# Optimization experiments

Measured on AMD Instinct MI355X. Metric: run time of the kernel, lower is better.

Reference implementation:

```python
import jax, jax.numpy as jnp
import numpy as np

K = 20
EPS = 1e-5
NEG_SLOPE = 0.2


def _knn(x):
    # x: (B, C, N) -> idx of K nearest (largest negative sq dist): (B, N, K)
    inner = -2.0 * jnp.einsum('bcn,bcm->bnm', x, x)
    xx = jnp.sum(x * x, axis=1)  # (B, N)
    pd = -xx[:, :, None] - inner - xx[:, None, :]
    return jax.lax.top_k(pd, K)[1]


def _graph_feature(x):
    # x: (B, C, N) -> (B, 2C, N, K) edge features cat(nbr - center, center)
    idx = _knn(x)                              # (B, N, K)
    xt = jnp.swapaxes(x, 1, 2)                 # (B, N, C)
    nbr = jax.vmap(lambda f, i: f[i])(xt, idx)  # (B, N, K, C)
    center = xt[:, :, None, :]
    feat = jnp.concatenate([nbr - center, jnp.broadcast_to(center, nbr.shape)], axis=-1)
    return jnp.transpose(feat, (0, 3, 1, 2))


def _bn(x, g, b, m, v):
    # inference-mode batchnorm over channel axis 1
    shp = [1] * x.ndim
    shp[1] = -1
    scale = (g / jnp.sqrt(v + EPS)).reshape(shp)
    return (x - m.reshape(shp)) * scale + b.reshape(shp)


def _lrelu(x):
    return jnp.where(x >= 0, x, NEG_SLOPE * x)


def setup_inputs() -> dict:
    key = jax.random.key(0)
    ks = jax.random.split(key, 16)
    d = {
        'x': jax.random.normal(ks[0], (4, 2, 4096), jnp.float32),
        'W1': jax.random.normal(ks[1], (64, 4), jnp.float32),
        'g1': jax.random.uniform(ks[2], (64,), jnp.float32),
        'b1': jax.random.normal(ks[3], (64,), jnp.float32),
        'm1': jnp.zeros((64,), jnp.float32),
        'v1': jnp.ones((64,), jnp.float32),
        'W2': jax.random.normal(ks[4], (64, 128), jnp.float32),
        'g2': jax.random.uniform(ks[5], (64,), jnp.float32),
        'b2': jax.random.normal(ks[6], (64,), jnp.float32),
        'm2': jnp.zeros((64,), jnp.float32),
        'v2': jnp.ones((64,), jnp.float32),
        'W5': jax.random.normal(ks[7], (128, 128), jnp.float32),
        'g5': jax.random.uniform(ks[8], (128,), jnp.float32),
        'b5': jax.random.normal(ks[9], (128,), jnp.float32),
        'm5': jnp.zeros((128,), jnp.float32),
        'v5': jnp.ones((128,), jnp.float32),
        'W6': jax.random.normal(ks[10], (256, 256), jnp.float32),
        'g6': jax.random.uniform(ks[11], (256,), jnp.float32),
        'b6': jax.random.normal(ks[12], (256,), jnp.float32),
        'm6': jnp.zeros((256,), jnp.float32),
        'v6': jnp.ones((256,), jnp.float32),
        'W9': jax.random.normal(ks[13], (1, 256), jnp.float32),
    }
    return d


def reference(x, W1, g1, b1, m1, v1, W2, g2, b2, m2, v2,
              W5, g5, b5, m5, v5, W6, g6, b6, m6, v6, W9):
    B, _, N = x.shape
    # EdgeConv 1
    f = _graph_feature(x)                                     # (B, 4, N, K)
    h = _lrelu(_bn(jnp.einsum('bcnk,oc->bonk', f, W1), g1, b1, m1, v1))
    x1 = jnp.max(h, axis=-1)                                  # (B, 64, N)
    # EdgeConv 2 (graph rebuilt in feature space)
    f = _graph_feature(x1)                                    # (B, 128, N, K)
    h = _lrelu(_bn(jnp.einsum('bcnk,oc->bonk', f, W2), g2, b2, m2, v2))
    x2 = jnp.max(h, axis=-1)                                  # (B, 64, N)
    xc = jnp.concatenate([x1, x2], axis=1)                    # (B, 128, N)
    # conv5 (1x1 conv1d) + global max pool
    h5 = _lrelu(_bn(jnp.einsum('bcn,oc->bon', xc, W5), g5, b5, m5, v5))  # (B, 128, N)
    gmax = jnp.max(h5, axis=-1)                               # (B, 128)
    rep = jnp.broadcast_to(gmax[:, :, None], (B, gmax.shape[1], N))
    cat = jnp.concatenate([rep, xc], axis=1)                  # (B, 256, N)
    # conv6 (dropout is identity in eval) then conv9
    h6 = _lrelu(_bn(jnp.einsum('bcn,oc->bon', cat, W6), g6, b6, m6, v6))
    out = jnp.einsum('bcn,oc->bon', h6, W9)                   # (B, 1, N)
    return out.reshape(B, N)
```

## Files before the change

### kernel.cpp

```cpp
#include <hip/hip_runtime.h>
#include <math.h>

#define NEGINF (-INFINITY)
constexpr int Np = 4096;
constexpr int Kn = 20;
constexpr float EPSf = 1e-5f;
constexpr float SLOPE = 0.2f;

typedef __bf16 bf16x8 __attribute__((ext_vector_type(8)));
typedef float f32x4 __attribute__((ext_vector_type(4)));
typedef unsigned long long ull;
typedef unsigned int u32;
typedef unsigned short u16;

__global__ __launch_bounds__(512, 2) void k1_knn1_edge1(
    const float* __restrict__ x, const float* __restrict__ W1,
    const float* __restrict__ g1, const float* __restrict__ b1,
    const float* __restrict__ m1, const float* __restrict__ v1,
    float* __restrict__ x1, __bf16* __restrict__ x1h, __bf16* __restrict__ x1l,
    float* __restrict__ xx2)
{
  __shared__ u32 smem32[16000];
  float* pk1  = (float*)smem32;
  u16*   pi1  = (u16*)((char*)smem32 + 32768);
  u32*   thrK = (u32*)((char*)smem32 + 49152);
  u32*   ku   = smem32;
  u16*   ki   = (u16*)((char*)smem32 + 40960);
  u16*   midx = (u16*)((char*)smem32 + 61440);
  float* nbr  = (float*)smem32;

  const int b = blockIdx.y;
  const int n0 = blockIdx.x * 64;
  const int tid = threadIdx.x;
  const int w = tid >> 6, L = tid & 63;
  const float* __restrict__ xr = x + (size_t)b*2*Np;
  const float* __restrict__ yr = xr + Np;

  const int n = n0 + L;
  const float px = xr[n], py = yr[n];

  if (tid < 64) thrK[tid] = 0xFFFFFFFFu;
  __syncthreads();

  ull kv[20];
#pragma unroll
  for (int s = 0; s < 20; ++s) kv[s] = 0ull;
  u32 u_cut = 0xFFFFFFFFu;
  int cnt = 0;

  auto flushK = [&]() {
#pragma unroll 1
    for (int f0 = 0; f0 < 16; f0 += 4) {
      if (__all(f0 >= cnt)) break;
      float fv[4]; u32 ji[4];
#pragma unroll
      for (int u = 0; u < 4; ++u) {
        fv[u] = pk1[(f0+u)*512 + tid];
        ji[u] = pi1[(f0+u)*512 + tid];
      }
#pragma unroll
      for (int u = 0; u < 4; ++u) {
        int f = f0 + u;
        ull key = (((ull)(~__float_as_uint(fv[u]))) << 32) | (u32)~ji[u];
        if (f < cnt && key > kv[19]) {
          ull ck = key;
#pragma unroll
          for (int s = 0; s < 20; ++s) {
            bool sw = ck > kv[s];
            ull tv = kv[s];
            kv[s] = sw ? ck : kv[s];
            ck = sw ? tv : ck;
          }
        }
      }
    }
    cnt = 0;
    u32 uc = ~(u32)(kv[19] >> 32);
    atomicMin(&thrK[L], uc);
    u_cut = thrK[L];
  };

  const int base = w * 512;
#pragma unroll 1
  for (int j0 = base; j0 < base + 512; j0 += 16) {
    {
      u32 hs = thrK[L];
      u_cut = hs < u_cut ? hs : u_cut;
    }
#pragma unroll
    for (int c = 0; c < 4; ++c) {
      float4 xv = *reinterpret_cast<const float4*>(xr + j0 + c*4);
      float4 yv = *reinterpret_cast<const float4*>(yr + j0 + c*4);
      const float xs[4] = {xv.x, xv.y, xv.z, xv.w};
      const float ys[4] = {yv.x, yv.y, yv.z, yv.w};
#pragma unroll
      for (int r = 0; r < 4; ++r) {
        float dx = xs[r] - px, dy = ys[r] - py;
        float s = dx*dx + dy*dy;
        u32 ub = __float_as_uint(s);
        if (ub <= u_cut) {
          pk1[cnt*512 + tid] = s;
          pi1[cnt*512 + tid] = (u16)(j0 + c*4 + r);
          ++cnt;
        }
      }
      if (__any(cnt >= 13)) flushK();
    }
  }
  flushK();

  __syncthreads();
#pragma unroll
  for (int k = 0; k < Kn; ++k) {
    ku[((size_t)w*64 + L)*20 + k] = (u32)(kv[k] >> 32);
    ki[((size_t)w*64 + L)*20 + k] = (u16)~(u32)kv[k];
  }
  __syncthreads();

  if (tid < 64) {
    const int p = tid;
    u32 hk_[8]; u16 hj_[8]; int pc[8];
#pragma unroll
    for (int q = 0; q < 8; ++q) {
      size_t bi = ((size_t)q*64 + p)*20;
      hk_[q] = ku[bi]; hj_[q] = ki[bi]; pc[q] = 0;
    }
    for (int k = 0; k < Kn; ++k) {
      u32 bk = hk_[0]; u16 bj = hj_[0]; int sel = 0;
#pragma unroll
      for (int q = 1; q < 8; ++q) {
        bool better = (hk_[q] > bk) || (hk_[q] == bk && hj_[q] < bj);
        if (better) { bk = hk_[q]; bj = hj_[q]; sel = q; }
      }
      midx[p*20 + k] = bj;
      int np_ = ++pc[sel];
      size_t bi = ((size_t)sel*64 + p)*20;
      hk_[sel] = (np_ < 20) ? ku[bi + np_] : 0u;
      hj_[sel] = (np_ < 20) ? ki[bi + np_] : (u16)0xFFFF;
    }
  }
  __syncthreads();

  for (int i = tid; i < 64*Kn; i += 512) {
    int j = midx[i];
    nbr[i*2]     = xr[j];
    nbr[i*2 + 1] = yr[j];
  }
  __syncthreads();

  const int o = L;
  const float4 w1v = reinterpret_cast<const float4*>(W1)[o];
  const float sc = g1[o] / sqrtf(v1[o] + EPSf);
  const float mo = m1[o], bo = b1[o];

  for (int pi = 0; pi < 8; ++pi) {
    const int p = w*8 + pi;
    const int np = n0 + p;
    const float cx0 = xr[np], cx1 = yr[np];
    const float cterm = (w1v.z - w1v.x)*cx0 + (w1v.w - w1v.y)*cx1;
    float xm = NEGINF;
#pragma unroll
    for (int k = 0; k < Kn; ++k) {
      float2 nv = *reinterpret_cast<const float2*>(&nbr[(p*20 + k)*2]);
      float vv = w1v.x*nv.x + w1v.y*nv.y + cterm;
      float h = (vv - mo)*sc + bo;
      h = h >= 0.f ? h : SLOPE*h;
      xm = fmaxf(xm, h);
    }
    x1[(b*64 + o)*Np + np] = xm;
    __bf16 hb = (__bf16)xm;
    __bf16 lb = (__bf16)(xm - (float)hb);
    size_t tbase = ((size_t)b*Np + np)*64 + o;
    x1h[tbase] = hb;
    x1l[tbase] = lb;
    float s = xm*xm;
#pragma unroll
    for (int off = 1; off < 64; off <<= 1) s += __shfl_xor(s, off);
    if (L == 0) xx2[b*Np + np] = s;
  }
}

__global__ __launch_bounds__(256, 2) void k2_knn2(
    const __bf16* __restrict__ xh, const __bf16* __restrict__ xl,
    const float* __restrict__ xx2, int* __restrict__ idx2)
{
  __shared__ ull smem[5120];
  float* sxx = (float*)smem;
  float* pk  = (float*)((char*)smem + 16384);
  u16*   pi  = (u16*)((char*)smem + 31744);
  u32*   thr = (u32*)((char*)smem + 39424);

  const int b = blockIdx.y;
  const int n0 = blockIdx.x * 16;
  const int tid = threadIdx.x;
  const int w = tid >> 6, L = tid & 63;
  const int L15 = L & 15, quad = L >> 4;

  for (int j = tid*4; j < Np; j += 1024)
    *reinterpret_cast<float4*>(&sxx[j]) = *reinterpret_cast<const float4*>(&xx2[(size_t)b*Np + j]);
  if (tid < 16) thr[tid] = 0u;

  const __bf16* Rh = xh + ((size_t)b*Np + n0)*64;
  const __bf16* Rl = xl + ((size_t)b*Np + n0)*64;
  bf16x8 rh0 = *reinterpret_cast<const bf16x8*>(Rh + L15*64 +  0 + quad*8);
  bf16x8 rh1 = *reinterpret_cast<const bf16x8*>(Rh + L15*64 + 32 + quad*8);
  bf16x8 rl0 = *reinterpret_cast<const bf16x8*>(Rl + L15*64 +  0 + quad*8);
  bf16x8 rl1 = *reinterpret_cast<const bf16x8*>(Rl + L15*64 + 32 + quad*8);

  const __bf16* Cbh = xh + (size_t)b*Np*64;
  const __bf16* Cbl = xl + (size_t)b*Np*64;

  ull kv[20];
#pragma unroll
  for (int s = 0; s < 20; ++s) kv[s] = 0ull;
  float fthresh = NEGINF;
  int cnt = 0;

  __syncthreads();

  auto flush = [&]() {
#pragma unroll 1
    for (int f0 = 0; f0 < 15; f0 += 4) {
      if (__all(f0 >= cnt)) break;
      float fv[4]; u32 ji[4];
#pragma unroll
      for (int u = 0; u < 4; ++u) {
        fv[u] = pk[(f0+u)*256 + tid];
        ji[u] = pi[(f0+u)*256 + tid];
      }
#pragma unroll
      for (int u = 0; u < 4; ++u) {
        int f = f0 + u;
        u32 uu = __float_as_uint(fv[u]);
        u32 hk = uu ^ ((u32)((int)uu >> 31) | 0x80000000u);
        ull key = (((ull)hk) << 32) | (u32)~ji[u];
        if (f < cnt && key > kv[19]) {
          ull ck = key;
#pragma unroll
          for (int s = 0; s < 20; ++s) {
            bool sw = ck > kv[s];
            ull tv = kv[s];
            kv[s] = sw ? ck : kv[s];
            ck = sw ? tv : ck;
          }
        }
      }
    }
    cnt = 0;
    ull t = kv[19];
    ull t2 = __shfl_xor(t, 16); t = t2 > t ? t2 : t;
    t2 = __shfl_xor(t, 32);     t = t2 > t ? t2 : t;
    if (t != 0ull && quad == 0) atomicMax(&thr[L15], (u32)(t >> 32));
    u32 hs = thr[L15];
    if (hs != 0u) {
      u32 u = (hs >> 31) ? (hs ^ 0x80000000u) : ~hs;
      fthresh = fmaxf(fthresh, __uint_as_float(u));
    }
  };

#pragma unroll 1
  for (int t = 0; t < 16; ++t) {
    {
      u32 hs = thr[L15];
      if (hs != 0u) {
        u32 u = (hs >> 31) ? (hs ^ 0x80000000u) : ~hs;
        fthresh = fmaxf(fthresh, __uint_as_float(u));
      }
    }
    const int tt = w + t*4;
    const int colbase = tt * 64;
    const __bf16* ph = Cbh + (size_t)colbase*64;
    const __bf16* pl = Cbl + (size_t)colbase*64;
    bf16x8 AH[4][2], AL[4][2];
#pragma unroll
    for (int s = 0; s < 4; ++s) {
      AH[s][0] = *reinterpret_cast<const bf16x8*>(ph + (s*16 + L15)*64 +  0 + quad*8);
      AH[s][1] = *reinterpret_cast<const bf16x8*>(ph + (s*16 + L15)*64 + 32 + quad*8);
      AL[s][0] = *reinterpret_cast<const bf16x8*>(pl + (s*16 + L15)*64 +  0 + quad*8);
      AL[s][1] = *reinterpret_cast<const bf16x8*>(pl + (s*16 + L15)*64 + 32 + quad*8);
    }

    f32x4 acc[4];
#pragma unroll
    for (int s = 0; s < 4; ++s) {
      acc[s] = (f32x4){0.f, 0.f, 0.f, 0.f};
      acc[s] = __builtin_amdgcn_mfma_f32_16x16x32_bf16(AH[s][0], rh0, acc[s], 0, 0, 0);
      acc[s] = __builtin_amdgcn_mfma_f32_16x16x32_bf16(AH[s][1], rh1, acc[s], 0, 0, 0);
      acc[s] = __builtin_amdgcn_mfma_f32_16x16x32_bf16(AH[s][0], rl0, acc[s], 0, 0, 0);
      acc[s] = __builtin_amdgcn_mfma_f32_16x16x32_bf16(AH[s][1], rl1, acc[s], 0, 0, 0);
      acc[s] = __builtin_amdgcn_mfma_f32_16x16x32_bf16(AL[s][0], rh0, acc[s], 0, 0, 0);
      acc[s] = __builtin_amdgcn_mfma_f32_16x16x32_bf16(AL[s][1], rh1, acc[s], 0, 0, 0);
    }

#pragma unroll
    for (int s = 0; s < 4; ++s) {
      float4 xv = *reinterpret_cast<const float4*>(&sxx[colbase + s*16 + quad*4]);
      const float xvr[4] = {xv.x, xv.y, xv.z, xv.w};
#pragma unroll
      for (int r = 0; r < 4; ++r) {
        float e = 2.0f*acc[s][r] - xvr[r];
        if (e >= fthresh) {
          pk[cnt*256 + tid] = e;
          pi[cnt*256 + tid] = (u16)(colbase + s*16 + quad*4 + r);
          ++cnt;
        }
      }
      if (__any(cnt >= 12)) flush();
    }
  }
  flush();

  __syncthreads();
#pragma unroll
  for (int k = 0; k < Kn; ++k) smem[((size_t)w*64 + L)*20 + k] = kv[k];
  __syncthreads();

  if (tid < 16) {
    const int r = tid;
    ull h[16]; int pc[16];
#pragma unroll
    for (int i = 0; i < 16; ++i) {
      h[i] = smem[((size_t)(i>>2)*64 + (i&3)*16 + r)*20];
      pc[i] = 0;
    }
    size_t obase = ((size_t)b*Np + n0 + r)*Kn;
    for (int k = 0; k < Kn; ++k) {
      ull best = h[0]; int sel = 0;
#pragma unroll
      for (int i = 1; i < 16; ++i) if (h[i] > best) { best = h[i]; sel = i; }
      idx2[obase + k] = (int)~(u32)best;
      int np_ = ++pc[sel];
      h[sel] = (np_ < 20) ? smem[((size_t)(sel>>2)*64 + (sel&3)*16 + r)*20 + np_] : 0ull;
    }
  }
}

__global__ __launch_bounds__(256) void kY(
    const __bf16* __restrict__ xh, const __bf16* __restrict__ xl,
    const float* __restrict__ W2,
    const float* __restrict__ g2, const float* __restrict__ b2,
    const float* __restrict__ m2, const float* __restrict__ v2,
    float* __restrict__ Za, float* __restrict__ Cn)
{
  __shared__ float w2t[128*66];
  const int b = blockIdx.y;
  const int n0 = blockIdx.x * 16;
  const int tid = threadIdx.x;
  const int w = tid >> 6, L = tid & 63;

  for (int i = tid; i < 8192; i += 256) {
    int o = i >> 7, c = i & 127;
    w2t[c*66 + o] = W2[i];
  }
  __syncthreads();

  const float sc = g2[L] / sqrtf(v2[L] + EPSf);
  const float cc = b2[L] - m2[L]*sc;

  for (int pi = 0; pi < 4; ++pi) {
    const int n = n0 + w*4 + pi;
    const size_t base = ((size_t)b*Np + n)*64;
    const float xv = (float)xh[base + L] + (float)xl[base + L];
    float ya = 0.f, yb = 0.f;
#pragma unroll
    for (int c = 0; c < 64; ++c) {
      float xc = __shfl(xv, c);
      ya += w2t[c*66 + L] * xc;
      yb += w2t[(64 + c)*66 + L] * xc;
    }
    float za = sc * ya;
    Za[base + L] = za;
    Cn[base + L] = sc * yb + cc - za;
  }
}

__global__ __launch_bounds__(256, 2) void k3_gather(
    const float* __restrict__ Za, const float* __restrict__ Cn,
    const int* __restrict__ idx2, float* __restrict__ x2)
{
  const int b = blockIdx.y;
  const int tid = threadIdx.x;
  const int w = tid >> 6, L = tid & 63;
  const int n = blockIdx.x*4 + w;

  const int* ip = idx2 + ((size_t)b*Np + n)*Kn;
  int jreg = (L < Kn) ? ip[L] : 0;
  const float c = Cn[((size_t)b*Np + n)*64 + L];
  float xm = NEGINF;
#pragma unroll
  for (int k = 0; k < Kn; ++k) {
    int j = __shfl(jreg, k);
    float hh = Za[((size_t)b*Np + j)*64 + L] + c;
    hh = hh >= 0.f ? hh : SLOPE*hh;
    xm = fmaxf(xm, hh);
  }
  x2[(b*64 + L)*Np + n] = xm;
}

__global__ __launch_bounds__(512) void k4_conv5max(
    const float* __restrict__ x1, const float* __restrict__ x2,
    const float* __restrict__ W5,
    const float* __restrict__ g5, const float* __restrict__ b5,
    const float* __restrict__ m5, const float* __restrict__ v5,
    float* __restrict__ partials)
{
  const int b = blockIdx.y, nb = blockIdx.x;
  const int tid = threadIdx.x;
  const int p = tid & 63;
  const int g = __builtin_amdgcn_readfirstlane(tid >> 6);
  const int n = nb*64 + p;
  float xcr[128];
#pragma unroll
  for (int c = 0; c < 64; ++c) {
    xcr[c]    = x1[(b*64 + c)*Np + n];
    xcr[64+c] = x2[(b*64 + c)*Np + n];
  }
  for (int oi = 0; oi < 16; ++oi) {
    const int o = g*16 + oi;
    const float* wr = W5 + o*128;
    float dot = 0.f;
#pragma unroll
    for (int c = 0; c < 128; c += 4) {
      float4 wv = *reinterpret_cast<const float4*>(wr + c);
      dot += wv.x*xcr[c] + wv.y*xcr[c+1] + wv.z*xcr[c+2] + wv.w*xcr[c+3];
    }
    float hv = (dot - m5[o])*(g5[o]/sqrtf(v5[o]+EPSf)) + b5[o];
    hv = hv >= 0.f ? hv : SLOPE*hv;
#pragma unroll
    for (int off = 1; off < 64; off <<= 1) hv = fmaxf(hv, __shfl_xor(hv, off));
    if (p == 0) partials[(b*128 + o)*64 + nb] = hv;
  }
}

__global__ __launch_bounds__(256) void k5_reduce_t6(
    const float* __restrict__ partials, const float* __restrict__ W6,
    float* __restrict__ t6)
{
  __shared__ float sg[128];
  const int b = blockIdx.x;
  const int tid = threadIdx.x;
  if (tid < 128) {
    float m = NEGINF;
    for (int w = 0; w < 64; ++w) m = fmaxf(m, partials[(b*128 + tid)*64 + w]);
    sg[tid] = m;
  }
  __syncthreads();
  float a = 0.f;
#pragma unroll
  for (int c = 0; c < 128; c += 4) {
    float4 wv = *reinterpret_cast<const float4*>(W6 + tid*256 + c);
    a += wv.x*sg[c] + wv.y*sg[c+1] + wv.z*sg[c+2] + wv.w*sg[c+3];
  }
  t6[b*256 + tid] = a;
}

__global__ __launch_bounds__(512) void k6_conv6_out(
    const float* __restrict__ x1, const float* __restrict__ x2,
    const float* __restrict__ W6, const float* __restrict__ t6,
    const float* __restrict__ g6, const float* __restrict__ b6,
    const float* __restrict__ m6, const float* __restrict__ v6,
    const float* __restrict__ W9,
    float* __restrict__ out)
{
  __shared__ float red[8][64];
  const int b = blockIdx.y, nb = blockIdx.x;
  const int tid = threadIdx.x;
  const int p = tid & 63;
  const int g = __builtin_amdgcn_readfirstlane(tid >> 6);
  const int n = nb*64 + p;
  float xcr[128];
#pragma unroll
  for (int c = 0; c < 64; ++c) {
    xcr[c]    = x1[(b*64 + c)*Np + n];
    xcr[64+c] = x2[(b*64 + c)*Np + n];
  }
  float oacc = 0.f;
  for (int oi = 0; oi < 32; ++oi) {
    const int o = g*32 + oi;
    const float* wr = W6 + o*256 + 128;
    float dot = t6[b*256 + o];
#pragma unroll
    for (int c = 0; c < 128; c += 4) {
      float4 wv = *reinterpret_cast<const float4*>(wr + c);
      dot += wv.x*xcr[c] + wv.y*xcr[c+1] + wv.z*xcr[c+2] + wv.w*xcr[c+3];
    }
    float hv = (dot - m6[o])*(g6[o]/sqrtf(v6[o]+EPSf)) + b6[o];
    hv = hv >= 0.f ? hv : SLOPE*hv;
    oacc += W9[o]*hv;
  }
  red[g][p] = oacc;
  __syncthreads();
  if (tid < 64) {
    float s = 0.f;
#pragma unroll
    for (int q = 0; q < 8; ++q) s += red[q][tid];
    out[b*Np + nb*64 + tid] = s;
  }
}

extern "C" void kernel_launch(void* const* d_in, const int* in_sizes, int n_in,
                              void* d_out, int out_size, void* d_ws, size_t ws_size,
                              hipStream_t stream) {
  const float* x  = (const float*)d_in[0];
  const float* W1 = (const float*)d_in[1];
  const float* g1 = (const float*)d_in[2];
  const float* b1 = (const float*)d_in[3];
  const float* m1 = (const float*)d_in[4];
  const float* v1 = (const float*)d_in[5];
  const float* W2 = (const float*)d_in[6];
  const float* g2 = (const float*)d_in[7];
  const float* b2 = (const float*)d_in[8];
  const float* m2 = (const float*)d_in[9];
  const float* v2 = (const float*)d_in[10];
  const float* W5 = (const float*)d_in[11];
  const float* g5 = (const float*)d_in[12];
  const float* b5 = (const float*)d_in[13];
  const float* m5 = (const float*)d_in[14];
  const float* v5 = (const float*)d_in[15];
  const float* W6 = (const float*)d_in[16];
  const float* g6 = (const float*)d_in[17];
  const float* b6 = (const float*)d_in[18];
  const float* m6 = (const float*)d_in[19];
  const float* v6 = (const float*)d_in[20];
  const float* W9 = (const float*)d_in[21];
  float* out = (float*)d_out;

  float* F = (float*)d_ws;
  float*  x1    = F;
  float*  xx2   = F + 1048576;
  __bf16* x1h   = (__bf16*)(F + 1064960);
  __bf16* x1l   = (__bf16*)(F + 1589248);
  float*  x2    = F + 2113536;
  int*    idx2  = (int*)(F + 3162112);
  float*  t6    = F + 3489792;
  float*  parts = F + 3490816;
  float*  Za    = F + 3523584;
  float*  Cn    = F + 4572160;

  k1_knn1_edge1<<<dim3(64,4), 512, 0, stream>>>(x, W1, g1, b1, m1, v1, x1, x1h, x1l, xx2);
  k2_knn2<<<dim3(256,4), 256, 0, stream>>>(x1h, x1l, xx2, idx2);
  kY<<<dim3(256,4), 256, 0, stream>>>(x1h, x1l, W2, g2, b2, m2, v2, Za, Cn);
  k3_gather<<<dim3(1024,4), 256, 0, stream>>>(Za, Cn, idx2, x2);
  k4_conv5max<<<dim3(64,4), 512, 0, stream>>>(x1, x2, W5, g5, b5, m5, v5, parts);
  k5_reduce_t6<<<4, 256, 0, stream>>>(parts, W6, t6);
  k6_conv6_out<<<dim3(64,4), 512, 0, stream>>>(x1, x2, W6, t6, g6, b6, m6, v6, W9, out);
}
```

Baseline: 537.0 us.

## Halve points per block in kNN1 kernel and split candidates across sixteen slices

New measurement: 554.2 us. 3.2% more time.

```diff
diff --git a/kernel.cpp b/kernel.cpp
--- a/kernel.cpp
+++ b/kernel.cpp
@@ -13,7 +13,7 @@
 typedef unsigned int u32;
 typedef unsigned short u16;
 
-__global__ __launch_bounds__(512, 2) void k1_knn1_edge1(
+__global__ __launch_bounds__(512, 4) void k1_knn1_edge1(
     const float* __restrict__ x, const float* __restrict__ W1,
     const float* __restrict__ g1, const float* __restrict__ b1,
     const float* __restrict__ m1, const float* __restrict__ v1,
@@ -30,16 +30,18 @@
   float* nbr  = (float*)smem32;
 
   const int b = blockIdx.y;
-  const int n0 = blockIdx.x * 64;
+  const int n0 = blockIdx.x * 32;
   const int tid = threadIdx.x;
   const int w = tid >> 6, L = tid & 63;
+  const int p = L & 31;
+  const int q = tid >> 5;
   const float* __restrict__ xr = x + (size_t)b*2*Np;
   const float* __restrict__ yr = xr + Np;
 
-  const int n = n0 + L;
+  const int n = n0 + p;
   const float px = xr[n], py = yr[n];
 
-  if (tid < 64) thrK[tid] = 0xFFFFFFFFu;
+  if (tid < 32) thrK[tid] = 0xFFFFFFFFu;
   __syncthreads();
 
   ull kv[20];
@@ -76,15 +78,15 @@
     }
     cnt = 0;
     u32 uc = ~(u32)(kv[19] >> 32);
-    atomicMin(&thrK[L], uc);
-    u_cut = thrK[L];
+    atomicMin(&thrK[p], uc);
+    u_cut = thrK[p];
   };
 
-  const int base = w * 512;
+  const int base = q * 256;
 #pragma unroll 1
-  for (int j0 = base; j0 < base + 512; j0 += 16) {
+  for (int j0 = base; j0 < base + 256; j0 += 16) {
     {
-      u32 hs = thrK[L];
+      u32 hs = thrK[p];
       u_cut = hs < u_cut ? hs : u_cut;
     }
 #pragma unroll
@@ -112,36 +114,36 @@
   __syncthreads();
 #pragma unroll
   for (int k = 0; k < Kn; ++k) {
-    ku[((size_t)w*64 + L)*20 + k] = (u32)(kv[k] >> 32);
-    ki[((size_t)w*64 + L)*20 + k] = (u16)~(u32)kv[k];
-  }
-  __syncthreads();
-
-  if (tid < 64) {
-    const int p = tid;
-    u32 hk_[8]; u16 hj_[8]; int pc[8];
-#pragma unroll
-    for (int q = 0; q < 8; ++q) {
-      size_t bi = ((size_t)q*64 + p)*20;
-      hk_[q] = ku[bi]; hj_[q] = ki[bi]; pc[q] = 0;
+    ku[((size_t)q*32 + p)*20 + k] = (u32)(kv[k] >> 32);
+    ki[((size_t)q*32 + p)*20 + k] = (u16)~(u32)kv[k];
+  }
+  __syncthreads();
+
+  if (tid < 32) {
+    const int pp = tid;
+    u32 hk_[16]; u16 hj_[16]; int pc[16];
+#pragma unroll
+    for (int i = 0; i < 16; ++i) {
+      size_t bi = ((size_t)i*32 + pp)*20;
+      hk_[i] = ku[bi]; hj_[i] = ki[bi]; pc[i] = 0;
     }
     for (int k = 0; k < Kn; ++k) {
       u32 bk = hk_[0]; u16 bj = hj_[0]; int sel = 0;
 #pragma unroll
-      for (int q = 1; q < 8; ++q) {
-        bool better = (hk_[q] > bk) || (hk_[q] == bk && hj_[q] < bj);
-        if (better) { bk = hk_[q]; bj = hj_[q]; sel = q; }
-      }
-      midx[p*20 + k] = bj;
+      for (int i = 1; i < 16; ++i) {
+        bool better = (hk_[i] > bk) || (hk_[i] == bk && hj_[i] < bj);
+        if (better) { bk = hk_[i]; bj = hj_[i]; sel = i; }
+      }
+      midx[pp*20 + k] = bj;
       int np_ = ++pc[sel];
-      size_t bi = ((size_t)sel*64 + p)*20;
+      size_t bi = ((size_t)sel*32 + pp)*20;
       hk_[sel] = (np_ < 20) ? ku[bi + np_] : 0u;
       hj_[sel] = (np_ < 20) ? ki[bi + np_] : (u16)0xFFFF;
     }
   }
   __syncthreads();
 
-  for (int i = tid; i < 64*Kn; i += 512) {
+  for (int i = tid; i < 32*Kn; i += 512) {
     int j = midx[i];
     nbr[i*2]     = xr[j];
     nbr[i*2 + 1] = yr[j];
@@ -153,15 +155,15 @@
   const float sc = g1[o] / sqrtf(v1[o] + EPSf);
   const float mo = m1[o], bo = b1[o];
 
-  for (int pi = 0; pi < 8; ++pi) {
-    const int p = w*8 + pi;
-    const int np = n0 + p;
+  for (int pi = 0; pi < 4; ++pi) {
+    const int pp = w*4 + pi;
+    const int np = n0 + pp;
     const float cx0 = xr[np], cx1 = yr[np];
     const float cterm = (w1v.z - w1v.x)*cx0 + (w1v.w - w1v.y)*cx1;
     float xm = NEGINF;
 #pragma unroll
     for (int k = 0; k < Kn; ++k) {
-      float2 nv = *reinterpret_cast<const float2*>(&nbr[(p*20 + k)*2]);
+      float2 nv = *reinterpret_cast<const float2*>(&nbr[(pp*20 + k)*2]);
       float vv = w1v.x*nv.x + w1v.y*nv.y + cterm;
       float h = (vv - mo)*sc + bo;
       h = h >= 0.f ? h : SLOPE*h;
@@ -440,8 +442,13 @@
   const int b = blockIdx.x;
   const int tid = threadIdx.x;
   if (tid < 128) {
+    const float4* pr = reinterpret_cast<const float4*>(partials + ((size_t)b*128 + tid)*64);
     float m = NEGINF;
-    for (int w = 0; w < 64; ++w) m = fmaxf(m, partials[(b*128 + tid)*64 + w]);
+#pragma unroll
+    for (int w = 0; w < 16; ++w) {
+      float4 v = pr[w];
+      m = fmaxf(m, fmaxf(fmaxf(v.x, v.y), fmaxf(v.z, v.w)));
+    }
     sg[tid] = m;
   }
   __syncthreads();
@@ -537,7 +544,7 @@
   float*  Za    = F + 3523584;
   float*  Cn    = F + 4572160;
 
-  k1_knn1_edge1<<<dim3(64,4), 512, 0, stream>>>(x, W1, g1, b1, m1, v1, x1, x1h, x1l, xx2);
+  k1_knn1_edge1<<<dim3(128,4), 512, 0, stream>>>(x, W1, g1, b1, m1, v1, x1, x1h, x1l, xx2);
   k2_knn2<<<dim3(256,4), 256, 0, stream>>>(x1h, x1l, xx2, idx2);
   kY<<<dim3(256,4), 256, 0, stream>>>(x1h, x1l, W2, g2, b2, m2, v2, Za, Cn);
   k3_gather<<<dim3(1024,4), 256, 0, stream>>>(Za, Cn, idx2, x2);
```
